# Performance work log

Measured on AMD Instinct MI355X. Metric: run time of the kernel, lower is better.

Reference implementation:

```python
import math
import jax, jax.numpy as jnp
import numpy as np

EPS = 1e-12
INV_4PI = 1.0 / (4.0 * math.pi)
B, NF = 32768, 3
RES_THETA, RES_PHI = 21, 41


def _make_quadrature(res_theta, res_phi):
    theta = np.linspace(0.0, math.pi, res_theta, dtype=np.float32)
    phi = np.linspace(0.0, 2.0 * math.pi, res_phi, dtype=np.float32)
    tm = 0.5 * (theta[:-1] + theta[1:])
    pm = 0.5 * (phi[:-1] + phi[1:])
    dth = theta[1:] - theta[:-1]
    dph = phi[1:] - phi[:-1]
    st, ct = np.sin(tm), np.cos(tm)
    sp, cp = np.sin(pm), np.cos(pm)
    vx = np.outer(st, cp).reshape(-1)
    vy = np.outer(st, sp).reshape(-1)
    vz = np.outer(ct, np.ones_like(pm)).reshape(-1)
    w = np.outer(st * dth, dph).reshape(-1)
    return (jnp.asarray(vx), jnp.asarray(vy), jnp.asarray(vz), jnp.asarray(w))


def setup_inputs() -> dict:
    key = jax.random.key(0)
    k1, k2, k3 = jax.random.split(key, 3)
    # positive densities O(1), flux magnitude <= 0.9*N (physically valid moments)
    dens = jax.random.uniform(k1, (B, 2, NF), minval=0.3, maxval=1.0, dtype=jnp.float32)
    fdir = jax.random.normal(k2, (B, 2, NF, 3), dtype=jnp.float32)
    fdir = fdir / jnp.clip(jnp.linalg.norm(fdir, axis=-1, keepdims=True), 1e-6)
    fmag = jax.random.uniform(k3, (B, 2, NF), minval=0.0, maxval=0.9, dtype=jnp.float32)
    F = fdir * (dens * fmag)[..., None]
    F4_in = jnp.concatenate([F, dens[..., None]], axis=-1)  # [B,2,NF,4]
    dir_x, dir_y, dir_z, quad_w = _make_quadrature(RES_THETA, RES_PHI)
    return {"F4_in": F4_in, "dir_x": dir_x, "dir_y": dir_y, "dir_z": dir_z, "quad_w": quad_w}


def _z_approxbis(f):
    f = jnp.clip(f, 0.0, 0.999999)
    f2 = f * f
    f4 = f2 * f2
    f6 = f4 * f2
    f8 = f4 * f4
    denom = 3.0 - 1.00651 * f2 - 0.962251 * f4 + 1.47353 * f6 - 0.48953 * f8
    p = 1.0 - 2.0 * (1.0 - f) * (1.0 + 1.01524 * f) / jnp.clip(denom, EPS)
    return 2.0 * f / jnp.clip(1.0 - p, 1e-06)


def _z_over_sinh_z(z):
    small = jnp.abs(z) < 1e-4
    zs = jnp.where(small, 1.0, z)  # avoid 0/0 in unused branch
    series = 1.0 - z * z / 6.0 + (z * z) * (z * z) / 120.0
    return jnp.where(small, series, zs / jnp.sinh(zs))


def _forward(F4_in, dir_x, dir_y, dir_z, quad_w):
    nf = F4_in.shape[2]
    N_e, N_ebar = F4_in[:, 0, 0, 3], F4_in[:, 1, 0, 3]
    F_e, F_ebar = F4_in[:, 0, 0, :3], F4_in[:, 1, 0, :3]
    if nf > 1:
        N_x = jnp.mean(F4_in[:, 0, 1:, 3], axis=1)
        N_xbar = jnp.mean(F4_in[:, 1, 1:, 3], axis=1)
        F_x = jnp.mean(F4_in[:, 0, 1:, :3], axis=1)
        F_xbar = jnp.mean(F4_in[:, 1, 1:, :3], axis=1)
    else:
        N_x, N_xbar, F_x, F_xbar = N_e, N_ebar, F_e, F_ebar
    N = jnp.clip(jnp.stack([N_e, N_ebar, N_x, N_xbar], axis=1), EPS)  # [B,4]
    F = jnp.stack([F_e, F_ebar, F_x, F_xbar], axis=1)  # [B,4,3]
    normF = jnp.sqrt(jnp.sum(F * F, axis=2))  # [B,4]
    fluxfac = jnp.clip(normF / N, 0.0, 0.999999)
    Z = _z_approxbis(fluxfac)  # [B,4]
    # mu: projection of unit direction onto flux direction, [B,4,D]
    mu = (F[:, :, 0, None] * dir_x + F[:, :, 1, None] * dir_y + F[:, :, 2, None] * dir_z) / jnp.clip(normF[..., None], EPS)
    g = N[..., None] * INV_4PI * _z_over_sinh_z(Z)[..., None] * jnp.exp(Z[..., None] * mu)  # [B,4,D]
    gnue, gnuebar, gnux, gnuxbar = g[:, 0], g[:, 1], g[:, 2], g[:, 3]
    delta = gnue - gnuebar - gnux + gnuxbar  # [B,D]
    Hpos = (delta >= 0.0).astype(g.dtype)
    Hneg = 1.0 - Hpos
    Iplus = jnp.sum(quad_w * jnp.maximum(delta, 0.0), axis=1)  # [B]
    Iminus = jnp.sum(quad_w * jnp.maximum(-delta, 0.0), axis=1)
    Ip_s = jnp.clip(Iplus, EPS)
    Im_s = jnp.clip(Iminus, EPS)
    third = jnp.full_like(Iplus, 1.0 / 3.0)
    coeff_pos = jnp.clip(jnp.where(Iplus < Iminus, third, 1.0 - 2.0 / 3.0 * (Im_s / Ip_s)), 0.0, 1.0)
    coeff_neg = jnp.clip(jnp.where(Iplus < Iminus, 1.0 - 2.0 / 3.0 * (Ip_s / Im_s), third), 0.0, 1.0)
    Psur = coeff_pos[:, None] * Hpos + coeff_neg[:, None] * Hneg  # [B,D]
    gnue_t = gnue * Psur + gnux * (1.0 - Psur)
    gnuebar_t = gnuebar * Psur + gnuxbar * (1.0 - Psur)
    gnux_t = 0.5 * (1.0 - Psur) * gnue + 0.5 * (1.0 + Psur) * gnux
    gnuxbar_t = 0.5 * (1.0 - Psur) * gnuebar + 0.5 * (1.0 + Psur) * gnuxbar
    g_t = jnp.stack([gnue_t, gnuebar_t, gnux_t, gnuxbar_t], axis=1)  # [B,4,D]
    gw = g_t * quad_w  # [B,4,D]
    newN = jnp.sum(gw, axis=2)  # [B,4]
    newF = jnp.stack([jnp.sum(gw * dir_x, axis=2), jnp.sum(gw * dir_y, axis=2), jnp.sum(gw * dir_z, axis=2)], axis=2)  # [B,4,3]
    b = F4_in.shape[0]
    if nf > 1:
        F_nu = jnp.concatenate([newF[:, 0:1], jnp.broadcast_to(newF[:, 2:3], (b, nf - 1, 3))], axis=1)
        F_nubar = jnp.concatenate([newF[:, 1:2], jnp.broadcast_to(newF[:, 3:4], (b, nf - 1, 3))], axis=1)
        N_nu = jnp.concatenate([newN[:, 0:1], jnp.broadcast_to(newN[:, 2:3], (b, nf - 1))], axis=1)
        N_nubar = jnp.concatenate([newN[:, 1:2], jnp.broadcast_to(newN[:, 3:4], (b, nf - 1))], axis=1)
    else:
        F_nu, F_nubar = newF[:, 0:1], newF[:, 1:2]
        N_nu, N_nubar = newN[:, 0:1], newN[:, 1:2]
    nu = jnp.concatenate([F_nu, N_nu[..., None]], axis=-1)  # [B,NF,4]
    nubar = jnp.concatenate([F_nubar, N_nubar[..., None]], axis=-1)
    F4mix = jnp.stack([nu, nubar], axis=1)  # [B,2,NF,4]
    growth = jnp.sqrt(jnp.clip(Iplus * Iminus, 0.0))
    return (F4mix, growth)


def reference(F4_in, dir_x, dir_y, dir_z, quad_w):
    return _forward(F4_in, dir_x, dir_y, dir_z, quad_w)
```

## Files before the change

kernel.cpp:

```cpp
#include <hip/hip_runtime.h>
#include <math.h>

#define EPSF     1e-12f
#define INV_4PI  0.07957747154594767f
#define LOG2E    1.4426950408889634f

typedef float v2f __attribute__((ext_vector_type(2)));

#if __has_builtin(__builtin_elementwise_fma)
#define FMA2(a, b, c) __builtin_elementwise_fma((a), (b), (c))
#else
#define FMA2(a, b, c) ((a) * (b) + (c))
#endif
#if __has_builtin(__builtin_elementwise_max)
#define MAX2(a, b) __builtin_elementwise_max((a), (b))
#else
static __device__ __forceinline__ v2f MAX2(v2f a, v2f b) {
    v2f r; r.x = fmaxf(a.x, b.x); r.y = fmaxf(a.y, b.y); return r;
}
#endif

#define EXP2(x) __builtin_amdgcn_exp2f(x)

__device__ __forceinline__ float zapprox(float f) {
    float f2 = f * f;
    float f4 = f2 * f2;
    float f6 = f4 * f2;
    float f8 = f4 * f4;
    float denom = 3.0f - 1.00651f * f2 - 0.962251f * f4 + 1.47353f * f6 - 0.48953f * f8;
    denom = fmaxf(denom, EPSF);
    float p = 1.0f - 2.0f * (1.0f - f) * (1.0f + 1.01524f * f) / denom;
    return 2.0f * f / fmaxf(1.0f - p, 1e-6f);
}

__device__ __forceinline__ float z_over_sinh(float z) {
    float zz = z * z;
    float series = 1.0f - zz / 6.0f + zz * zz / 120.0f;
    float E = __expf(z);
    float s = 0.5f * (E - 1.0f / E);
    float r = z / s;
    return (z < 1e-4f) ? series : r;
}

struct Spec { float zx, zy, zz, la; };

__device__ __forceinline__ Spec setup_spec(float N, float Fx, float Fy, float Fz) {
    N = fmaxf(N, EPSF);
    float nf = sqrtf(Fx * Fx + Fy * Fy + Fz * Fz);
    float f  = fminf(fmaxf(nf / N, 0.0f), 0.999999f);
    float Z  = zapprox(f);
    float A  = N * INV_4PI * z_over_sinh(Z);
    float sc = Z * LOG2E / fmaxf(nf, EPSF);
    Spec s;
    s.zx = Fx * sc; s.zy = Fy * sc; s.zz = Fz * sc;
    s.la = log2f(A);
    return s;
}

__device__ __forceinline__ v2f bcast(float x) { v2f r; r.x = x; r.y = x; return r; }

__global__ __launch_bounds__(256, 2) void box3d_kernel(
    const float* __restrict__ F4,
    const float* __restrict__ dxp, const float* __restrict__ dyp,
    const float* __restrict__ dzp, const float* __restrict__ qwp,
    float* __restrict__ out, int B, int ndir)
{
    __shared__ float sqx[800], sqy[800], sqz[800], sqw[800];
    for (int d = threadIdx.x; d < ndir; d += blockDim.x) {
        sqx[d] = dxp[d]; sqy[d] = dyp[d]; sqz[d] = dzp[d]; sqw[d] = qwp[d];
    }
    __syncthreads();

    const int sub = threadIdx.x & 15;
    const int grp = threadIdx.x >> 4;
    const int b = blockIdx.x * 16 + grp;
    if (b >= B) return;

    const float4* row = (const float4*)(F4 + (size_t)b * 24);
    float4 r0 = row[0], r1 = row[1], r2 = row[2];
    float4 r3 = row[3], r4 = row[4], r5 = row[5];

    Spec s0 = setup_spec(r0.w, r0.x, r0.y, r0.z);
    Spec s1 = setup_spec(r3.w, r3.x, r3.y, r3.z);
    Spec s2 = setup_spec(0.5f * (r1.w + r2.w), 0.5f * (r1.x + r2.x),
                         0.5f * (r1.y + r2.y), 0.5f * (r1.z + r2.z));
    Spec s3 = setup_spec(0.5f * (r4.w + r5.w), 0.5f * (r4.x + r5.x),
                         0.5f * (r4.y + r5.y), 0.5f * (r4.z + r5.z));

    v2f zx0 = bcast(s0.zx), zy0 = bcast(s0.zy), zz0 = bcast(s0.zz), la0 = bcast(s0.la);
    v2f zx1 = bcast(s1.zx), zy1 = bcast(s1.zy), zz1 = bcast(s1.zz), la1 = bcast(s1.la);
    v2f zx2 = bcast(s2.zx), zy2 = bcast(s2.zy), zz2 = bcast(s2.zz), la2 = bcast(s2.la);
    v2f zx3 = bcast(s3.zx), zy3 = bcast(s3.zy), zz3 = bcast(s3.zz), la3 = bcast(s3.la);

    const v2f zero = bcast(0.0f);
    v2f aip = zero, aim = zero;
    v2f aut0 = zero, aut1 = zero, aut2 = zero, aut3 = zero;
    v2f aup0 = zero, aup1 = zero, aup2 = zero, aup3 = zero;
    v2f avt0 = zero, avt1 = zero, avt2 = zero, avt3 = zero;
    v2f avp0 = zero, avp1 = zero, avp2 = zero, avp3 = zero;
    v2f agx0 = zero, agx1 = zero, agx2 = zero, agx3 = zero;
    v2f agy0 = zero, agy1 = zero, agy2 = zero, agy3 = zero;

    const int npair = ndir >> 1;
    for (int p = sub; p < npair; p += 16) {
        int d0 = p * 2;
        v2f qx = *(const v2f*)&sqx[d0];
        v2f qy = *(const v2f*)&sqy[d0];
        v2f qz = *(const v2f*)&sqz[d0];
        v2f qw = *(const v2f*)&sqw[d0];

        v2f t0 = FMA2(zx0, qx, FMA2(zy0, qy, FMA2(zz0, qz, la0)));
        v2f t1 = FMA2(zx1, qx, FMA2(zy1, qy, FMA2(zz1, qz, la1)));
        v2f t2 = FMA2(zx2, qx, FMA2(zy2, qy, FMA2(zz2, qz, la2)));
        v2f t3 = FMA2(zx3, qx, FMA2(zy3, qy, FMA2(zz3, qz, la3)));
        v2f g0, g1, g2, g3;
        g0.x = EXP2(t0.x); g0.y = EXP2(t0.y);
        g1.x = EXP2(t1.x); g1.y = EXP2(t1.y);
        g2.x = EXP2(t2.x); g2.y = EXP2(t2.y);
        g3.x = EXP2(t3.x); g3.y = EXP2(t3.y);

        v2f u = g0 - g2, v = g1 - g3;
        v2f wu = qw * u, wv = qw * v;
        v2f wd = wu - wv;
        aip += MAX2(wd, zero);
        aim += MAX2(-wd, zero);

        v2f wup, wvp;
        wup.x = (wd.x >= 0.0f) ? wu.x : 0.0f;
        wup.y = (wd.y >= 0.0f) ? wu.y : 0.0f;
        wvp.x = (wd.x >= 0.0f) ? wv.x : 0.0f;
        wvp.y = (wd.y >= 0.0f) ? wv.y : 0.0f;
        v2f w2 = qw * g2, w3 = qw * g3;

        aut0 += wu;  aup0 += wup;  avt0 += wv;  avp0 += wvp;  agx0 += w2;  agy0 += w3;
        aut1 = FMA2(wu, qx, aut1);  aup1 = FMA2(wup, qx, aup1);
        avt1 = FMA2(wv, qx, avt1);  avp1 = FMA2(wvp, qx, avp1);
        agx1 = FMA2(w2, qx, agx1);  agy1 = FMA2(w3, qx, agy1);
        aut2 = FMA2(wu, qy, aut2);  aup2 = FMA2(wup, qy, aup2);
        avt2 = FMA2(wv, qy, avt2);  avp2 = FMA2(wvp, qy, avp2);
        agx2 = FMA2(w2, qy, agx2);  agy2 = FMA2(w3, qy, agy2);
        aut3 = FMA2(wu, qz, aut3);  aup3 = FMA2(wup, qz, aup3);
        avt3 = FMA2(wv, qz, avt3);  avp3 = FMA2(wvp, qz, avp3);
        agx3 = FMA2(w2, qz, agx3);  agy3 = FMA2(w3, qz, agy3);
    }

    float ip  = aip.x + aip.y,   im  = aim.x + aim.y;
    float ut0 = aut0.x + aut0.y, ut1 = aut1.x + aut1.y, ut2 = aut2.x + aut2.y, ut3 = aut3.x + aut3.y;
    float up0 = aup0.x + aup0.y, up1 = aup1.x + aup1.y, up2 = aup2.x + aup2.y, up3 = aup3.x + aup3.y;
    float vt0 = avt0.x + avt0.y, vt1 = avt1.x + avt1.y, vt2 = avt2.x + avt2.y, vt3 = avt3.x + avt3.y;
    float vp0 = avp0.x + avp0.y, vp1 = avp1.x + avp1.y, vp2 = avp2.x + avp2.y, vp3 = avp3.x + avp3.y;
    float gx0 = agx0.x + agx0.y, gx1 = agx1.x + agx1.y, gx2 = agx2.x + agx2.y, gx3 = agx3.x + agx3.y;
    float gy0 = agy0.x + agy0.y, gy1 = agy1.x + agy1.y, gy2 = agy2.x + agy2.y, gy3 = agy3.x + agy3.y;

    #pragma unroll
    for (int msk = 1; msk <= 8; msk <<= 1) {
        ip  += __shfl_xor(ip,  msk);  im  += __shfl_xor(im,  msk);
        ut0 += __shfl_xor(ut0, msk);  ut1 += __shfl_xor(ut1, msk);
        ut2 += __shfl_xor(ut2, msk);  ut3 += __shfl_xor(ut3, msk);
        up0 += __shfl_xor(up0, msk);  up1 += __shfl_xor(up1, msk);
        up2 += __shfl_xor(up2, msk);  up3 += __shfl_xor(up3, msk);
        vt0 += __shfl_xor(vt0, msk);  vt1 += __shfl_xor(vt1, msk);
        vt2 += __shfl_xor(vt2, msk);  vt3 += __shfl_xor(vt3, msk);
        vp0 += __shfl_xor(vp0, msk);  vp1 += __shfl_xor(vp1, msk);
        vp2 += __shfl_xor(vp2, msk);  vp3 += __shfl_xor(vp3, msk);
        gx0 += __shfl_xor(gx0, msk);  gx1 += __shfl_xor(gx1, msk);
        gx2 += __shfl_xor(gx2, msk);  gx3 += __shfl_xor(gx3, msk);
        gy0 += __shfl_xor(gy0, msk);  gy1 += __shfl_xor(gy1, msk);
        gy2 += __shfl_xor(gy2, msk);  gy3 += __shfl_xor(gy3, msk);
    }

    float Ips = fmaxf(ip, EPSF), Ims = fmaxf(im, EPSF);
    const float third = 1.0f / 3.0f;
    float cp, cn;
    if (ip < im) {
        cp = third;
        cn = fminf(fmaxf(1.0f - (2.0f / 3.0f) * (Ips / Ims), 0.0f), 1.0f);
    } else {
        cp = fminf(fmaxf(1.0f - (2.0f / 3.0f) * (Ims / Ips), 0.0f), 1.0f);
        cn = third;
    }

    float P0 = cp * up0 + cn * (ut0 - up0), Q0 = cp * vp0 + cn * (vt0 - vp0);
    float P1 = cp * up1 + cn * (ut1 - up1), Q1 = cp * vp1 + cn * (vt1 - vp1);
    float P2 = cp * up2 + cn * (ut2 - up2), Q2 = cp * vp2 + cn * (vt2 - vp2);
    float P3 = cp * up3 + cn * (ut3 - up3), Q3 = cp * vp3 + cn * (vt3 - vp3);

    float4* o4 = (float4*)out + (size_t)b * 6;
    if (sub == 0) {
        o4[0] = make_float4(gx1 + P1, gx2 + P2, gx3 + P3, gx0 + P0);
    } else if (sub == 1) {
        o4[1] = make_float4(gx1 + 0.5f * (ut1 - P1), gx2 + 0.5f * (ut2 - P2),
                            gx3 + 0.5f * (ut3 - P3), gx0 + 0.5f * (ut0 - P0));
    } else if (sub == 2) {
        o4[2] = make_float4(gx1 + 0.5f * (ut1 - P1), gx2 + 0.5f * (ut2 - P2),
                            gx3 + 0.5f * (ut3 - P3), gx0 + 0.5f * (ut0 - P0));
    } else if (sub == 3) {
        o4[3] = make_float4(gy1 + Q1, gy2 + Q2, gy3 + Q3, gy0 + Q0);
    } else if (sub == 4) {
        o4[4] = make_float4(gy1 + 0.5f * (vt1 - Q1), gy2 + 0.5f * (vt2 - Q2),
                            gy3 + 0.5f * (vt3 - Q3), gy0 + 0.5f * (vt0 - Q0));
    } else if (sub == 5) {
        o4[5] = make_float4(gy1 + 0.5f * (vt1 - Q1), gy2 + 0.5f * (vt2 - Q2),
                            gy3 + 0.5f * (vt3 - Q3), gy0 + 0.5f * (vt0 - Q0));
    } else if (sub == 6) {
        out[(size_t)B * 24 + b] = sqrtf(fmaxf(ip * im, 0.0f));
    }
}

extern "C" void kernel_launch(void* const* d_in, const int* in_sizes, int n_in,
                              void* d_out, int out_size, void* d_ws, size_t ws_size,
                              hipStream_t stream) {
    const float* F4 = (const float*)d_in[0];
    const float* dx = (const float*)d_in[1];
    const float* dy = (const float*)d_in[2];
    const float* dz = (const float*)d_in[3];
    const float* qw = (const float*)d_in[4];
    float* out = (float*)d_out;

    int B = in_sizes[0] / 24;
    int ndir = in_sizes[1];
    int blocks = (B + 15) / 16;
    box3d_kernel<<<blocks, 256, 0, stream>>>(F4, dx, dy, dz, qw, out, B, ndir);
}
```

Baseline: 105.2 us.

## Precompute spectral params in separate kernel and derive I+/I- from accumulated sums

Moves the per-row setup (zapprox, sinh, log2) into a separate spec_kernel that runs one thread per spectrum and writes float4 parameters to workspace. Previously each of the 16 lanes in a group computed all four setups redundantly. The main kernel now reads those parameters and raises its occupancy hint from 2 to 3. It also drops the Iplus/Iminus accumulators and shuffles, recovering them algebraically from up0-vp0 and ut0-vt0. The cost is an extra kernel launch and a workspace round trip.

```diff
diff --git a/kernel.cpp b/kernel.cpp
--- a/kernel.cpp
+++ b/kernel.cpp
@@ -11,13 +11,6 @@
 #define FMA2(a, b, c) __builtin_elementwise_fma((a), (b), (c))
 #else
 #define FMA2(a, b, c) ((a) * (b) + (c))
-#endif
-#if __has_builtin(__builtin_elementwise_max)
-#define MAX2(a, b) __builtin_elementwise_max((a), (b))
-#else
-static __device__ __forceinline__ v2f MAX2(v2f a, v2f b) {
-    v2f r; r.x = fmaxf(a.x, b.x); r.y = fmaxf(a.y, b.y); return r;
-}
 #endif
 
 #define EXP2(x) __builtin_amdgcn_exp2f(x)
@@ -42,25 +35,44 @@
     return (z < 1e-4f) ? series : r;
 }
 
-struct Spec { float zx, zy, zz, la; };
-
-__device__ __forceinline__ Spec setup_spec(float N, float Fx, float Fy, float Fz) {
+__device__ __forceinline__ float4 setup_spec(float N, float Fx, float Fy, float Fz) {
     N = fmaxf(N, EPSF);
     float nf = sqrtf(Fx * Fx + Fy * Fy + Fz * Fz);
     float f  = fminf(fmaxf(nf / N, 0.0f), 0.999999f);
     float Z  = zapprox(f);
     float A  = N * INV_4PI * z_over_sinh(Z);
     float sc = Z * LOG2E / fmaxf(nf, EPSF);
-    Spec s;
-    s.zx = Fx * sc; s.zy = Fy * sc; s.zz = Fz * sc;
-    s.la = log2f(A);
-    return s;
+    return make_float4(Fx * sc, Fy * sc, Fz * sc, log2f(A));
+}
+
+__global__ __launch_bounds__(256) void spec_kernel(
+    const float* __restrict__ F4, float4* __restrict__ ws, int B)
+{
+    int t = blockIdx.x * blockDim.x + threadIdx.x;
+    if (t >= 4 * B) return;
+    int b = t >> 2, s = t & 3;
+    const float4* row = (const float4*)(F4 + (size_t)b * 24);
+    float N, Fx, Fy, Fz;
+    if (s == 0) {
+        float4 a = row[0];  N = a.w; Fx = a.x; Fy = a.y; Fz = a.z;
+    } else if (s == 1) {
+        float4 a = row[3];  N = a.w; Fx = a.x; Fy = a.y; Fz = a.z;
+    } else if (s == 2) {
+        float4 a = row[1], c = row[2];
+        N = 0.5f * (a.w + c.w); Fx = 0.5f * (a.x + c.x);
+        Fy = 0.5f * (a.y + c.y); Fz = 0.5f * (a.z + c.z);
+    } else {
+        float4 a = row[4], c = row[5];
+        N = 0.5f * (a.w + c.w); Fx = 0.5f * (a.x + c.x);
+        Fy = 0.5f * (a.y + c.y); Fz = 0.5f * (a.z + c.z);
+    }
+    ws[(size_t)b * 4 + s] = setup_spec(N, Fx, Fy, Fz);
 }
 
 __device__ __forceinline__ v2f bcast(float x) { v2f r; r.x = x; r.y = x; return r; }
 
-__global__ __launch_bounds__(256, 2) void box3d_kernel(
-    const float* __restrict__ F4,
+__global__ __launch_bounds__(256, 3) void box3d_kernel(
+    const float4* __restrict__ ws,
     const float* __restrict__ dxp, const float* __restrict__ dyp,
     const float* __restrict__ dzp, const float* __restrict__ qwp,
     float* __restrict__ out, int B, int ndir)
@@ -76,24 +88,14 @@
     const int b = blockIdx.x * 16 + grp;
     if (b >= B) return;
 
-    const float4* row = (const float4*)(F4 + (size_t)b * 24);
-    float4 r0 = row[0], r1 = row[1], r2 = row[2];
-    float4 r3 = row[3], r4 = row[4], r5 = row[5];
-
-    Spec s0 = setup_spec(r0.w, r0.x, r0.y, r0.z);
-    Spec s1 = setup_spec(r3.w, r3.x, r3.y, r3.z);
-    Spec s2 = setup_spec(0.5f * (r1.w + r2.w), 0.5f * (r1.x + r2.x),
-                         0.5f * (r1.y + r2.y), 0.5f * (r1.z + r2.z));
-    Spec s3 = setup_spec(0.5f * (r4.w + r5.w), 0.5f * (r4.x + r5.x),
-                         0.5f * (r4.y + r5.y), 0.5f * (r4.z + r5.z));
-
-    v2f zx0 = bcast(s0.zx), zy0 = bcast(s0.zy), zz0 = bcast(s0.zz), la0 = bcast(s0.la);
-    v2f zx1 = bcast(s1.zx), zy1 = bcast(s1.zy), zz1 = bcast(s1.zz), la1 = bcast(s1.la);
-    v2f zx2 = bcast(s2.zx), zy2 = bcast(s2.zy), zz2 = bcast(s2.zz), la2 = bcast(s2.la);
-    v2f zx3 = bcast(s3.zx), zy3 = bcast(s3.zy), zz3 = bcast(s3.zz), la3 = bcast(s3.la);
+    const float4* wsb = ws + (size_t)b * 4;
+    float4 f0 = wsb[0], f1 = wsb[1], f2 = wsb[2], f3 = wsb[3];
+    v2f zx0 = bcast(f0.x), zy0 = bcast(f0.y), zz0 = bcast(f0.z), la0 = bcast(f0.w);
+    v2f zx1 = bcast(f1.x), zy1 = bcast(f1.y), zz1 = bcast(f1.z), la1 = bcast(f1.w);
+    v2f zx2 = bcast(f2.x), zy2 = bcast(f2.y), zz2 = bcast(f2.z), la2 = bcast(f2.w);
+    v2f zx3 = bcast(f3.x), zy3 = bcast(f3.y), zz3 = bcast(f3.z), la3 = bcast(f3.w);
 
     const v2f zero = bcast(0.0f);
-    v2f aip = zero, aim = zero;
     v2f aut0 = zero, aut1 = zero, aut2 = zero, aut3 = zero;
     v2f aup0 = zero, aup1 = zero, aup2 = zero, aup3 = zero;
     v2f avt0 = zero, avt1 = zero, avt2 = zero, avt3 = zero;
@@ -121,15 +123,11 @@
 
         v2f u = g0 - g2, v = g1 - g3;
         v2f wu = qw * u, wv = qw * v;
-        v2f wd = wu - wv;
-        aip += MAX2(wd, zero);
-        aim += MAX2(-wd, zero);
-
         v2f wup, wvp;
-        wup.x = (wd.x >= 0.0f) ? wu.x : 0.0f;
-        wup.y = (wd.y >= 0.0f) ? wu.y : 0.0f;
-        wvp.x = (wd.x >= 0.0f) ? wv.x : 0.0f;
-        wvp.y = (wd.y >= 0.0f) ? wv.y : 0.0f;
+        wup.x = (u.x >= v.x) ? wu.x : 0.0f;
+        wup.y = (u.y >= v.y) ? wu.y : 0.0f;
+        wvp.x = (u.x >= v.x) ? wv.x : 0.0f;
+        wvp.y = (u.y >= v.y) ? wv.y : 0.0f;
         v2f w2 = qw * g2, w3 = qw * g3;
 
         aut0 += wu;  aup0 += wup;  avt0 += wv;  avp0 += wvp;  agx0 += w2;  agy0 += w3;
@@ -144,7 +142,6 @@
         agx3 = FMA2(w2, qz, agx3);  agy3 = FMA2(w3, qz, agy3);
     }
 
-    float ip  = aip.x + aip.y,   im  = aim.x + aim.y;
     float ut0 = aut0.x + aut0.y, ut1 = aut1.x + aut1.y, ut2 = aut2.x + aut2.y, ut3 = aut3.x + aut3.y;
     float up0 = aup0.x + aup0.y, up1 = aup1.x + aup1.y, up2 = aup2.x + aup2.y, up3 = aup3.x + aup3.y;
     float vt0 = avt0.x + avt0.y, vt1 = avt1.x + avt1.y, vt2 = avt2.x + avt2.y, vt3 = avt3.x + avt3.y;
@@ -154,7 +151,6 @@
 
     #pragma unroll
     for (int msk = 1; msk <= 8; msk <<= 1) {
-        ip  += __shfl_xor(ip,  msk);  im  += __shfl_xor(im,  msk);
         ut0 += __shfl_xor(ut0, msk);  ut1 += __shfl_xor(ut1, msk);
         ut2 += __shfl_xor(ut2, msk);  ut3 += __shfl_xor(ut3, msk);
         up0 += __shfl_xor(up0, msk);  up1 += __shfl_xor(up1, msk);
@@ -168,6 +164,9 @@
         gy0 += __shfl_xor(gy0, msk);  gy1 += __shfl_xor(gy1, msk);
         gy2 += __shfl_xor(gy2, msk);  gy3 += __shfl_xor(gy3, msk);
     }
+
+    float ip = fmaxf(up0 - vp0, 0.0f);
+    float im = fmaxf(ip - ut0 + vt0, 0.0f);
 
     float Ips = fmaxf(ip, EPSF), Ims = fmaxf(im, EPSF);
     const float third = 1.0f / 3.0f;
@@ -219,6 +218,10 @@
 
     int B = in_sizes[0] / 24;
     int ndir = in_sizes[1];
+    float4* ws = (float4*)d_ws;
+
+    int t1 = 4 * B;
+    spec_kernel<<<(t1 + 255) / 256, 256, 0, stream>>>(F4, ws, B);
     int blocks = (B + 15) / 16;
-    box3d_kernel<<<blocks, 256, 0, stream>>>(F4, dx, dy, dz, qw, out, B, ndir);
-}
+    box3d_kernel<<<blocks, 256, 0, stream>>>(ws, dx, dy, dz, qw, out, B, ndir);
+}
```

Result: faster. 96.37 us (-8.4%).
